# Kernel tuning notes

Hardware: AMD Instinct MI355X
Metric: run time of the kernel (lower is better)

## Reference

```python
import jax, jax.numpy as jnp
import numpy as np

B, DIM, T, H = 8, 1024, 2048, 16
HD = DIM // H  # per-head channel dim = 64


def _toeplitz(v):
    # v: (H, T) -> (H, T, T) with M[h, i, j] = v[h, j - i] if j >= i else 0
    m = v.shape[-1]
    i = jnp.arange(m)[:, None]
    j = jnp.arange(m)[None, :]
    idx = jnp.where(j >= i, j - i, 0)
    return jnp.where(j >= i, v[..., idx], jnp.zeros((), v.dtype))


def setup_inputs() -> dict:
    key = jax.random.key(0)
    ks = jax.random.split(key, 5)
    s = 1.0 / np.sqrt(DIM)
    return {
        "x": jax.random.normal(ks[0], (B, DIM, T), jnp.float32),
        "w_in": jax.random.normal(ks[1], (DIM, DIM), jnp.float32) * s,
        "b_in": jnp.zeros((DIM,), jnp.float32),
        "w_out": jax.random.normal(ks[2], (DIM, DIM), jnp.float32) * s,
        "b_out": jnp.zeros((DIM,), jnp.float32),
        "toep_w": jax.random.normal(ks[3], (H, T), jnp.float32) * 0.02,
        "toep_b": jnp.zeros((H, T), jnp.float32),
    }


def reference(x, w_in, b_in, w_out, b_out, toep_w, toep_b):
    # x: (B, DIM, T) -> (B, T, DIM)
    xt = jnp.transpose(x, (0, 2, 1))
    h1 = xt @ w_in.T + b_in  # (B, T, DIM)
    # (B, T, H*HD) -> (B, H, HD, T)
    p = jnp.transpose(h1.reshape(B, T, H, HD), (0, 2, 3, 1))
    M = _toeplitz(toep_w)  # (H, T, T)
    # bmm with per-head causal Toeplitz matrix + per-head bias over time
    conv = jnp.einsum("bhdt,htu->bhdu", p, M) + toep_b[None, :, None, :]
    # (B, H, HD, T) -> (B, T, H*HD)
    merged = jnp.transpose(conv, (0, 3, 1, 2)).reshape(B, T, DIM)
    out = merged @ w_out.T + b_out  # (B, T, DIM)
    return jnp.transpose(out, (0, 2, 1))  # (B, DIM, T)
```

## Files before the change

kernel.cpp:

```cpp
#include <hip/hip_runtime.h>
#include <hip/hip_bf16.h>
#include <stdint.h>

#define B_   8
#define DIM  1024
#define T_   2048
#define H_   16
#define HD   64

typedef __attribute__((ext_vector_type(8))) short bf16x8;
typedef __attribute__((ext_vector_type(4))) float f32x4;
typedef __attribute__((ext_vector_type(4))) unsigned short u16x4;

__device__ __forceinline__ unsigned short f2bf(float f) {
    union { float f; unsigned u; } v{f};
    unsigned r = v.u + 0x7fffu + ((v.u >> 16) & 1u);
    return (unsigned short)(r >> 16);
}

__device__ __forceinline__ void gl_lds16(const unsigned short* g, unsigned short* l) {
    __builtin_amdgcn_global_load_lds(
        (const __attribute__((address_space(1))) void*)(const void*)g,
        (__attribute__((address_space(3))) void*)(void*)l,
        16, 0, 0);
}

__device__ __forceinline__ bf16x8 ld_frag(const unsigned short* smem, int row, int cg) {
    return *reinterpret_cast<const bf16x8*>(smem + row * 64 + (((cg) ^ (row & 7)) << 3));
}

__global__ void xpose_cast(const float* __restrict__ x, unsigned short* __restrict__ xt) {
    __shared__ float tile[64][65];
    const int b = blockIdx.z;
    const int d0 = blockIdx.y * 64, t0 = blockIdx.x * 64;
    const int tid = threadIdx.x;
    const int c = tid & 63;
    const int r0 = tid >> 6;

    const float* xp = x + ((size_t)b * DIM + d0) * T_ + t0;
#pragma unroll
    for (int i = 0; i < 16; ++i) {
        int r = r0 + i * 4;
        tile[r][c] = xp[(size_t)r * T_ + c];
    }
    __syncthreads();
    unsigned short* op = xt + ((size_t)b * T_ + t0) * DIM + d0;
    const int ci = (tid & 15) * 4;
    const int rr = tid >> 4;
#pragma unroll
    for (int i = 0; i < 4; ++i) {
        int r = rr + i * 16;
        u16x4 v;
#pragma unroll
        for (int j = 0; j < 4; ++j) v[j] = f2bf(tile[ci + j][r]);
        *reinterpret_cast<u16x4*>(op + (size_t)r * DIM + ci) = v;
    }
}

__global__ void gen_mfrag(const float* __restrict__ tw, unsigned short* __restrict__ Mf) {
    const int h = blockIdx.y, dg = blockIdx.x;
    const int D = (dg - 1) * 64;
    const float* twh = tw + h * T_;
    unsigned short* out = Mf + (((size_t)h * 32 + dg) << 13);
    for (int v = threadIdx.x; v < 1024; v += 256) {
        int cg = v >> 7, row = v & 127;
        bf16x8 w;
#pragma unroll
        for (int j = 0; j < 8; ++j) {
            int lag = D + row - (cg * 8 + j);
            w[j] = (lag >= 0) ? (short)f2bf(twh[lag]) : (short)0;
        }
        *reinterpret_cast<bf16x8*>(out + (size_t)v * 8) = w;
    }
}

__global__ void gen_wfrag(const float* __restrict__ W, unsigned short* __restrict__ Wf) {
    const int kt = blockIdx.x, my = blockIdx.y;
    unsigned short* out = Wf + (((size_t)my * 16 + kt) << 13);
    for (int v = threadIdx.x; v < 1024; v += 256) {
        int cg = v >> 7, row = v & 127;
        const float* src = W + (size_t)(my * 128 + row) * DIM + kt * 64 + cg * 8;
        bf16x8 w;
#pragma unroll
        for (int j = 0; j < 8; ++j) w[j] = (short)f2bf(src[j]);
        *reinterpret_cast<bf16x8*>(out + (size_t)v * 8) = w;
    }
}

template <bool OUT_BF16>
__global__ void gemm3_k(const unsigned short* __restrict__ Wf,
                        const unsigned short* __restrict__ Bm,
                        const float* __restrict__ bias,
                        void* __restrict__ Out) {
    __shared__ __align__(16) unsigned short Bs[128 * 64];

    const int flat = blockIdx.x;
    const int wid  = (flat & 7) * 128 + (flat >> 3);
    const int nx   = wid & 15;
    const int my   = (wid >> 4) & 7;
    const int b    = wid >> 7;

    const int tid = threadIdx.x, lane = tid & 63, wv = tid >> 6;
    const int m0 = my * 128;
    const int n0 = nx * 128;
    const unsigned short* Bb = Bm + (size_t)b * T_ * DIM + (size_t)n0 * DIM;
    const unsigned short* Aw = Wf + (((size_t)my * 16) << 13);

    const int wr = wv >> 1, wc = wv & 1;
    const int lrow = lane & 15, lg = lane >> 4;
    const int rsub = lane >> 3;
    const int g = (lane & 7) ^ rsub;

    const int aoff = (lg * 128 + wr * 64 + lrow) * 8;

    f32x4 acc[4][4] = {};

    const int NT = DIM / 64;
    for (int kt = 0; kt < NT; ++kt) {
        __syncthreads();
        const unsigned short* At = Aw + ((size_t)kt << 13);
        bf16x8 af0[4], af1[4];
#pragma unroll
        for (int mt = 0; mt < 4; ++mt) {
            af0[mt] = *reinterpret_cast<const bf16x8*>(At + aoff + mt * 128);
            af1[mt] = *reinterpret_cast<const bf16x8*>(At + 4096 + aoff + mt * 128);
        }
        {
            const int k0 = kt * 64;
#pragma unroll
            for (int it = 0; it < 4; ++it) {
                int ch = wv * 4 + it;
                int r  = ch * 8 + rsub;
                gl_lds16(Bb + (size_t)r * DIM + k0 + g * 8, Bs + ch * 512);
            }
        }
        __syncthreads();

        bf16x8 bfr[4];
#pragma unroll
        for (int nt = 0; nt < 4; ++nt) bfr[nt] = ld_frag(Bs, wc * 64 + nt * 16 + lrow, lg);
#pragma unroll
        for (int mt = 0; mt < 4; ++mt)
#pragma unroll
            for (int nt = 0; nt < 4; ++nt)
                acc[mt][nt] = __builtin_amdgcn_mfma_f32_16x16x32_bf16(af0[mt], bfr[nt], acc[mt][nt], 0, 0, 0);
#pragma unroll
        for (int nt = 0; nt < 4; ++nt) bfr[nt] = ld_frag(Bs, wc * 64 + nt * 16 + lrow, 4 + lg);
#pragma unroll
        for (int mt = 0; mt < 4; ++mt)
#pragma unroll
            for (int nt = 0; nt < 4; ++nt)
                acc[mt][nt] = __builtin_amdgcn_mfma_f32_16x16x32_bf16(af1[mt], bfr[nt], acc[mt][nt], 0, 0, 0);
    }

    const size_t ob = (size_t)b * DIM * T_;
#pragma unroll
    for (int mt = 0; mt < 4; ++mt) {
        int d = m0 + wr * 64 + mt * 16 + lg * 4;
#pragma unroll
        for (int nt = 0; nt < 4; ++nt) {
            int t = n0 + wc * 64 + nt * 16 + lrow;
#pragma unroll
            for (int r = 0; r < 4; ++r) {
                float v = acc[mt][nt][r] + bias[d + r];
                if constexpr (OUT_BF16)
                    ((unsigned short*)Out)[ob + (size_t)(d + r) * T_ + t] = f2bf(v);
                else
                    ((float*)Out)[ob + (size_t)(d + r) * T_ + t] = v;
            }
        }
    }
}

__global__ void conv4_k(const unsigned short* __restrict__ H1,
                        const unsigned short* __restrict__ Mf,
                        const float* __restrict__ tb,
                        unsigned short* __restrict__ Cb) {
    __shared__ __align__(16) unsigned short Ps[2][64 * 64];

    const int flat = blockIdx.x;
    const int wid  = (flat & 7) * 128 + (flat >> 3);
    const int bx   = wid & 7;
    const int b    = (wid >> 3) & 7;
    const int h    = wid >> 6;

    const int tid = threadIdx.x, lane = tid & 63, wv = tid >> 6;
    const unsigned short* Hb = H1 + ((size_t)b * DIM + h * HD) * T_;
    const unsigned short* Ah = Mf + ((size_t)h * 32) * 8192;

    const int lrow = lane & 15, lg = lane >> 4;
    const int rsub = lane >> 3;
    const int g = (lane & 7) ^ rsub;

    const int aoff = (lg * 128 + wv * 32 + lrow) * 8;

#pragma unroll
    for (int ph = 0; ph < 2; ++ph) {
        const int ut = ph ? bx : (T_ / 128 - 1 - bx);
        const int u0 = ut * 128;
        const int nk = 2 * ut + 2;
        f32x4 acc[2][4] = {};

#pragma unroll
        for (int it = 0; it < 2; ++it) {
            int ch = wv * 2 + it;
            int r  = ch * 8 + rsub;
            gl_lds16(Hb + (size_t)r * T_ + g * 8, &Ps[0][0] + ch * 512);
        }
        __syncthreads();

        for (int kt = 0; kt < nk; ++kt) {
            const int cur = kt & 1;
            if (kt + 1 < nk) {
                const int t0n = (kt + 1) * 64;
#pragma unroll
                for (int it = 0; it < 2; ++it) {
                    int ch = wv * 2 + it;
                    int r  = ch * 8 + rsub;
                    gl_lds16(Hb + (size_t)r * T_ + t0n + g * 8, &Ps[cur ^ 1][0] + ch * 512);
                }
            }
            const int dg = 2 * ut - kt + 1;
            const unsigned short* At = Ah + (size_t)dg * 8192;
            bf16x8 af0[2], af1[2];
#pragma unroll
            for (int mt = 0; mt < 2; ++mt) {
                af0[mt] = *reinterpret_cast<const bf16x8*>(At + aoff + mt * 128);
                af1[mt] = *reinterpret_cast<const bf16x8*>(At + 4096 + aoff + mt * 128);
            }
            const unsigned short* Pb = &Ps[cur][0];
            bf16x8 bfr[4];
#pragma unroll
            for (int nt = 0; nt < 4; ++nt) bfr[nt] = ld_frag(Pb, nt * 16 + lrow, lg);
#pragma unroll
            for (int mt = 0; mt < 2; ++mt)
#pragma unroll
                for (int nt = 0; nt < 4; ++nt)
                    acc[mt][nt] = __builtin_amdgcn_mfma_f32_16x16x32_bf16(af0[mt], bfr[nt], acc[mt][nt], 0, 0, 0);
#pragma unroll
            for (int nt = 0; nt < 4; ++nt) bfr[nt] = ld_frag(Pb, nt * 16 + lrow, 4 + lg);
#pragma unroll
            for (int mt = 0; mt < 2; ++mt)
#pragma unroll
                for (int nt = 0; nt < 4; ++nt)
                    acc[mt][nt] = __builtin_amdgcn_mfma_f32_16x16x32_bf16(af1[mt], bfr[nt], acc[mt][nt], 0, 0, 0);

            __syncthreads();
        }

        const size_t base = (size_t)b * T_ * DIM + (size_t)h * HD;
#pragma unroll
        for (int mt = 0; mt < 2; ++mt) {
            int u = u0 + wv * 32 + mt * 16 + lg * 4;
            const float* tbp = tb + h * T_ + u;
            float t0v = tbp[0], t1v = tbp[1], t2v = tbp[2], t3v = tbp[3];
#pragma unroll
            for (int nt = 0; nt < 4; ++nt) {
                int d = nt * 16 + lrow;
                size_t p = base + (size_t)u * DIM + d;
                Cb[p]           = f2bf(acc[mt][nt][0] + t0v);
                Cb[p + DIM]     = f2bf(acc[mt][nt][1] + t1v);
                Cb[p + 2 * DIM] = f2bf(acc[mt][nt][2] + t2v);
                Cb[p + 3 * DIM] = f2bf(acc[mt][nt][3] + t3v);
            }
        }
    }
}

extern "C" void kernel_launch(void* const* d_in, const int* in_sizes, int n_in,
                              void* d_out, int out_size, void* d_ws, size_t ws_size,
                              hipStream_t stream) {
    (void)in_sizes; (void)n_in; (void)out_size; (void)ws_size;
    const float* x      = (const float*)d_in[0];
    const float* w_in   = (const float*)d_in[1];
    const float* b_in   = (const float*)d_in[2];
    const float* w_out  = (const float*)d_in[3];
    const float* b_out  = (const float*)d_in[4];
    const float* toep_w = (const float*)d_in[5];
    const float* toep_b = (const float*)d_in[6];

    char* ws = (char*)d_ws;
    unsigned short* XT    = (unsigned short*)(ws);
    unsigned short* H1    = (unsigned short*)(ws + 33554432);
    unsigned short* Cbuf  = (unsigned short*)(ws + 67108864);
    unsigned short* Mfrag = (unsigned short*)(ws + 100663296);
    unsigned short* WfI   = (unsigned short*)(ws + 109051904);
    unsigned short* WfO   = (unsigned short*)(ws + 111149056);

    xpose_cast<<<dim3(T_ / 64, DIM / 64, B_), dim3(256), 0, stream>>>(x, XT);
    gen_mfrag<<<dim3(32, H_), dim3(256), 0, stream>>>(toep_w, Mfrag);
    gen_wfrag<<<dim3(16, 8), dim3(256), 0, stream>>>(w_in, WfI);
    gen_wfrag<<<dim3(16, 8), dim3(256), 0, stream>>>(w_out, WfO);
    gemm3_k<true><<<dim3(1024), dim3(256), 0, stream>>>(WfI, XT, b_in, (void*)H1);
    conv4_k<<<dim3(1024), dim3(256), 0, stream>>>(H1, Mfrag, toep_b, Cbuf);
    gemm3_k<false><<<dim3(1024), dim3(256), 0, stream>>>(WfO, Cbuf, b_out, d_out);
}
```

Before: 181.1 us.

## Enlarge GEMM tile to 256x128 and double-buffer B tiles in LDS

The two projection GEMMs now compute a 256x128 output tile per block, with 128 rows per wave, so the grid shrinks to 512 blocks and each B tile loaded into LDS is reused across twice as many rows. The B tile is double-buffered: the async global-to-LDS load for the next k-step is issued before computing the current one, leaving one barrier per iteration instead of two. This raises accumulator register use to 128 floats per lane and doubles LDS use, so launch bounds of 2 blocks per CU are set. Lower occupancy and fewer blocks may hurt latency hiding.

```diff
diff --git a/kernel.cpp b/kernel.cpp
--- a/kernel.cpp
+++ b/kernel.cpp
@@ -88,75 +88,88 @@
 }
 
 template <bool OUT_BF16>
-__global__ void gemm3_k(const unsigned short* __restrict__ Wf,
-                        const unsigned short* __restrict__ Bm,
-                        const float* __restrict__ bias,
-                        void* __restrict__ Out) {
-    __shared__ __align__(16) unsigned short Bs[128 * 64];
+__global__ __launch_bounds__(256, 2)
+void gemm4_k(const unsigned short* __restrict__ Wf,
+             const unsigned short* __restrict__ Bm,
+             const float* __restrict__ bias,
+             void* __restrict__ Out) {
+    __shared__ __align__(16) unsigned short Bs[2][128 * 64];
 
     const int flat = blockIdx.x;
-    const int wid  = (flat & 7) * 128 + (flat >> 3);
+    const int wid  = (flat & 7) * 64 + (flat >> 3);
     const int nx   = wid & 15;
-    const int my   = (wid >> 4) & 7;
-    const int b    = wid >> 7;
+    const int mb   = (wid >> 4) & 3;
+    const int b    = wid >> 6;
 
     const int tid = threadIdx.x, lane = tid & 63, wv = tid >> 6;
-    const int m0 = my * 128;
+    const int wr = wv >> 1, wc = wv & 1;
     const int n0 = nx * 128;
-    const unsigned short* Bb = Bm + (size_t)b * T_ * DIM + (size_t)n0 * DIM;
-    const unsigned short* Aw = Wf + (((size_t)my * 16) << 13);
-
-    const int wr = wv >> 1, wc = wv & 1;
+    const unsigned short* Bb  = Bm + (size_t)b * T_ * DIM + (size_t)n0 * DIM;
+    const unsigned short* Awr = Wf + (((size_t)(mb * 2 + wr) * 16) << 13);
+
     const int lrow = lane & 15, lg = lane >> 4;
     const int rsub = lane >> 3;
     const int g = (lane & 7) ^ rsub;
 
-    const int aoff = (lg * 128 + wr * 64 + lrow) * 8;
-
-    f32x4 acc[4][4] = {};
+    const int aoff = (lg * 128 + lrow) * 8;
+
+    f32x4 acc[8][4] = {};
+
+    auto BSTAGE = [&](int kt, int p) {
+        const int k0 = kt * 64;
+#pragma unroll
+        for (int it = 0; it < 4; ++it) {
+            int ch = wv * 4 + it;
+            int r  = ch * 8 + rsub;
+            gl_lds16(Bb + (size_t)r * DIM + k0 + g * 8, &Bs[p][0] + ch * 512);
+        }
+    };
+
+    BSTAGE(0, 0);
+    __syncthreads();
 
     const int NT = DIM / 64;
     for (int kt = 0; kt < NT; ++kt) {
+        const int cur = kt & 1;
+        if (kt + 1 < NT) BSTAGE(kt + 1, cur ^ 1);
+
+        const unsigned short* At = Awr + ((size_t)kt << 13);
+        const unsigned short* Pb = &Bs[cur][0];
+
+        {
+            bf16x8 af[8], bfr[4];
+#pragma unroll
+            for (int mt = 0; mt < 8; ++mt)
+                af[mt] = *reinterpret_cast<const bf16x8*>(At + aoff + mt * 128);
+#pragma unroll
+            for (int nt = 0; nt < 4; ++nt) bfr[nt] = ld_frag(Pb, wc * 64 + nt * 16 + lrow, lg);
+#pragma unroll
+            for (int mt = 0; mt < 8; ++mt)
+#pragma unroll
+                for (int nt = 0; nt < 4; ++nt)
+                    acc[mt][nt] = __builtin_amdgcn_mfma_f32_16x16x32_bf16(af[mt], bfr[nt], acc[mt][nt], 0, 0, 0);
+        }
+        {
+            bf16x8 af[8], bfr[4];
+#pragma unroll
+            for (int mt = 0; mt < 8; ++mt)
+                af[mt] = *reinterpret_cast<const bf16x8*>(At + 4096 + aoff + mt * 128);
+#pragma unroll
+            for (int nt = 0; nt < 4; ++nt) bfr[nt] = ld_frag(Pb, wc * 64 + nt * 16 + lrow, 4 + lg);
+#pragma unroll
+            for (int mt = 0; mt < 8; ++mt)
+#pragma unroll
+                for (int nt = 0; nt < 4; ++nt)
+                    acc[mt][nt] = __builtin_amdgcn_mfma_f32_16x16x32_bf16(af[mt], bfr[nt], acc[mt][nt], 0, 0, 0);
+        }
+
         __syncthreads();
-        const unsigned short* At = Aw + ((size_t)kt << 13);
-        bf16x8 af0[4], af1[4];
-#pragma unroll
-        for (int mt = 0; mt < 4; ++mt) {
-            af0[mt] = *reinterpret_cast<const bf16x8*>(At + aoff + mt * 128);
-            af1[mt] = *reinterpret_cast<const bf16x8*>(At + 4096 + aoff + mt * 128);
-        }
-        {
-            const int k0 = kt * 64;
-#pragma unroll
-            for (int it = 0; it < 4; ++it) {
-                int ch = wv * 4 + it;
-                int r  = ch * 8 + rsub;
-                gl_lds16(Bb + (size_t)r * DIM + k0 + g * 8, Bs + ch * 512);
-            }
-        }
-        __syncthreads();
-
-        bf16x8 bfr[4];
-#pragma unroll
-        for (int nt = 0; nt < 4; ++nt) bfr[nt] = ld_frag(Bs, wc * 64 + nt * 16 + lrow, lg);
-#pragma unroll
-        for (int mt = 0; mt < 4; ++mt)
-#pragma unroll
-            for (int nt = 0; nt < 4; ++nt)
-                acc[mt][nt] = __builtin_amdgcn_mfma_f32_16x16x32_bf16(af0[mt], bfr[nt], acc[mt][nt], 0, 0, 0);
-#pragma unroll
-        for (int nt = 0; nt < 4; ++nt) bfr[nt] = ld_frag(Bs, wc * 64 + nt * 16 + lrow, 4 + lg);
-#pragma unroll
-        for (int mt = 0; mt < 4; ++mt)
-#pragma unroll
-            for (int nt = 0; nt < 4; ++nt)
-                acc[mt][nt] = __builtin_amdgcn_mfma_f32_16x16x32_bf16(af1[mt], bfr[nt], acc[mt][nt], 0, 0, 0);
     }
 
     const size_t ob = (size_t)b * DIM * T_;
 #pragma unroll
-    for (int mt = 0; mt < 4; ++mt) {
-        int d = m0 + wr * 64 + mt * 16 + lg * 4;
+    for (int mt = 0; mt < 8; ++mt) {
+        int d = mb * 256 + wr * 128 + mt * 16 + lg * 4;
 #pragma unroll
         for (int nt = 0; nt < 4; ++nt) {
             int t = n0 + wc * 64 + nt * 16 + lrow;
@@ -291,7 +304,7 @@
     gen_mfrag<<<dim3(32, H_), dim3(256), 0, stream>>>(toep_w, Mfrag);
     gen_wfrag<<<dim3(16, 8), dim3(256), 0, stream>>>(w_in, WfI);
     gen_wfrag<<<dim3(16, 8), dim3(256), 0, stream>>>(w_out, WfO);
-    gemm3_k<true><<<dim3(1024), dim3(256), 0, stream>>>(WfI, XT, b_in, (void*)H1);
+    gemm4_k<true><<<dim3(512), dim3(256), 0, stream>>>(WfI, XT, b_in, (void*)H1);
     conv4_k<<<dim3(1024), dim3(256), 0, stream>>>(H1, Mfrag, toep_b, Cbuf);
-    gemm3_k<false><<<dim3(1024), dim3(256), 0, stream>>>(WfO, Cbuf, b_out, d_out);
-}
+    gemm4_k<false><<<dim3(512), dim3(256), 0, stream>>>(WfO, Cbuf, b_out, d_out);
+}
```

Result: faster. 165.7 us (-8.5%).
